# Performance work log

Measured on AMD Instinct MI355X. Metric: run time of the kernel, lower is better.

Reference implementation:

```python
import jax, jax.numpy as jnp
import numpy as np

B_SZ, L_SEQ, D_DATA = 2, 1024, 8
D_CTRL = 256
POLY = 40
N_LAYERS = 2
D_STATE = 16
D_CONV = 4
D_INNER = 1 * D_CTRL          # expand_factor_control = 1
DT_RANK = -(-D_CTRL // 16)    # ceil(d_model/16) = 16
EPS = 1e-5


def setup_inputs() -> dict:
    key = jax.random.key(0)
    ks = jax.random.split(key, 12)
    s = 0.02
    x = jax.random.uniform(ks[0], (B_SZ, L_SEQ, D_DATA), dtype=jnp.float32)
    y = jax.random.uniform(ks[1], (B_SZ, L_SEQ, D_DATA), dtype=jnp.float32)
    return {
        'x': x,
        'y': y,
        # control_proj (note: fed 2*d_data features in structured forward)
        'control_proj_w': jax.random.normal(ks[2], (D_CTRL, 2 * D_DATA)) * s,
        'control_proj_b': jnp.zeros((D_CTRL,), jnp.float32),
        # stacked Mamba layer params (leading dim = n_layers)
        'norm_w': jnp.ones((N_LAYERS, D_CTRL), jnp.float32),
        'in_proj_w': jax.random.normal(ks[3], (N_LAYERS, 2 * D_INNER, D_CTRL)) * s,
        'conv_w': jax.random.normal(ks[4], (N_LAYERS, D_INNER, D_CONV)) * s,
        'conv_b': jnp.zeros((N_LAYERS, D_INNER), jnp.float32),
        'x_proj_w': jax.random.normal(ks[5], (N_LAYERS, DT_RANK + 2 * D_STATE, D_INNER)) * s,
        'dt_proj_w': jax.random.normal(ks[6], (N_LAYERS, D_INNER, DT_RANK)) * s,
        'dt_proj_b': jnp.zeros((N_LAYERS, D_INNER), jnp.float32),
        'A_log': jnp.tile(jnp.log(jnp.arange(1, D_STATE + 1, dtype=jnp.float32))[None, None, :], (N_LAYERS, D_INNER, 1)),
        'D_skip': jnp.ones((N_LAYERS, D_INNER), jnp.float32),
        'out_proj_w': jax.random.normal(ks[7], (N_LAYERS, D_CTRL, D_INNER)) * s,
        # b_net: Linear(d_control, 2*d_data*poly_dim^2)
        'b_net_w': jax.random.normal(ks[8], (2 * D_DATA * POLY * POLY, D_CTRL)) * s,
        'b_net_b': jnp.zeros((2 * D_DATA * POLY * POLY,), jnp.float32),
    }


def _rmsnorm(u, w):
    return u * jax.lax.rsqrt(jnp.mean(u * u, axis=-1, keepdims=True) + EPS) * w


def _causal_conv(u, w, b):
    # u: [B,L,C]; w: [C,K] depthwise causal conv, pad left K-1
    K = w.shape[-1]
    L = u.shape[1]
    up = jnp.pad(u, ((0, 0), (K - 1, 0), (0, 0)))
    acc = jnp.zeros_like(u)
    for k in range(K):  # K=4, fixed small kernel
        acc = acc + up[:, k:k + L, :] * w[:, k]
    return acc + b


def _mamba(u, norm_w, in_proj_w, conv_w, conv_b, x_proj_w, dt_proj_w, dt_proj_b, A_log, D_skip, out_proj_w):
    # mambapy-style stack of residual blocks: u = mixer(rmsnorm(u)) + u
    for i in range(N_LAYERS):
        r = _rmsnorm(u, norm_w[i])
        xz = jnp.einsum('bld,ed->ble', r, in_proj_w[i])          # [B,L,2*di]
        xc, zg = jnp.split(xz, 2, axis=-1)
        xc = jax.nn.silu(_causal_conv(xc, conv_w[i], conv_b[i]))  # [B,L,di]
        dbc = jnp.einsum('bld,ed->ble', xc, x_proj_w[i])          # [B,L,dt_rank+2*ds]
        delta = jax.nn.softplus(jnp.einsum('blr,dr->bld', dbc[..., :DT_RANK], dt_proj_w[i]) + dt_proj_b[i])
        Bm = dbc[..., DT_RANK:DT_RANK + D_STATE]
        Cm = dbc[..., DT_RANK + D_STATE:]
        A = -jnp.exp(A_log[i])                                    # [di,ds]
        dA = jnp.exp(delta[..., None] * A)                        # [B,L,di,ds]
        dBx = delta[..., None] * Bm[:, :, None, :] * xc[..., None]

        def step(h, inp):
            dA_t, dBx_t = inp
            h = dA_t * h + dBx_t
            return h, h

        h0 = jnp.zeros((u.shape[0], D_INNER, D_STATE), u.dtype)
        _, hs = jax.lax.scan(step, h0, (dA.transpose(1, 0, 2, 3), dBx.transpose(1, 0, 2, 3)))
        yv = jnp.einsum('lbds,lbs->bld', hs, Cm.transpose(1, 0, 2)) + D_skip[i] * xc
        yv = yv * jax.nn.silu(zg)
        u = jnp.einsum('bld,ed->ble', yv, out_proj_w[i]) + u
    return u


def _power_mat(z):
    # z ** arange(POLY), built with cumprod (grad-safe at exponent 0)
    ones = jnp.ones(z.shape + (1,), z.dtype)
    reps = jnp.broadcast_to(z[..., None], z.shape + (POLY - 1,))
    return jnp.cumprod(jnp.concatenate([ones, reps], axis=-1), axis=-1)  # [B,L,2d,P]


def reference(x, y, control_proj_w, control_proj_b, norm_w, in_proj_w, conv_w, conv_b,
              x_proj_w, dt_proj_w, dt_proj_b, A_log, D_skip, out_proj_w, b_net_w, b_net_b):
    B, L, d = x.shape
    xdot = y - x
    z = jnp.concatenate([x, xdot], axis=-1)                       # [B,L,2d]
    pm = _power_mat(z)                                            # [B,L,2d,P]
    ctrl_in = jnp.flip(jnp.concatenate([xdot, y], axis=-1), axis=1)
    ctrl_in = ctrl_in @ control_proj_w.T + control_proj_b
    sp = _mamba(ctrl_in, norm_w, in_proj_w, conv_w, conv_b, x_proj_w,
                dt_proj_w, dt_proj_b, A_log, D_skip, out_proj_w)
    state_pred = jnp.flip(sp, axis=1)                             # [B,L,d_ctrl]
    bmat = (state_pred @ b_net_w.T + b_net_b).reshape(B, L, 2 * d, POLY, POLY)
    pow1 = jnp.einsum('bldkj,bldk->bldj', bmat, pm)
    zdot = jnp.einsum('bldj,bldj->bld', pow1, jnp.flip(pm, axis=2))
    return zdot[:, 1:, :], state_pred
```

## Files before the change

### kernel.cpp

```cpp
#include <hip/hip_runtime.h>
#include <hip/hip_bf16.h>

#define B_SZ   2
#define LSEQ   1024
#define DD     8
#define DCTRL  256
#define POLY   40
#define NL     2
#define DSTATE 16
#define DCONV  4
#define DINNER 256
#define DTRANK 16
#define NBL    (B_SZ*LSEQ)
#define NROWS  (2*DD*POLY*POLY)
#define NSLOT  25
#define NCH    32
#define LCH    32
#define LDP    40

typedef __attribute__((ext_vector_type(8))) short bf16x8;
typedef __attribute__((ext_vector_type(8))) unsigned short us8;
typedef __attribute__((ext_vector_type(4))) unsigned short us4;
typedef __attribute__((ext_vector_type(4))) float f32x4;

__device__ __forceinline__ float sigmoidf_(float x){ return 1.f/(1.f+__expf(-x)); }
__device__ __forceinline__ float softplusf_(float x){ return fmaxf(x,0.f) + log1pf(__expf(-fabsf(x))); }
__device__ __forceinline__ unsigned short f2bf(float f){
  unsigned int u = __float_as_uint(f);
  unsigned int r = (u + 0x7fffu + ((u>>16)&1u)) >> 16;
  return (unsigned short)r;
}

__global__ void k_f2bf(const float* __restrict__ in, unsigned short* __restrict__ out, int n8){
  int i = blockIdx.x*blockDim.x + threadIdx.x;
  if (i>=n8) return;
  const float4* p = (const float4*)(in + (size_t)i*8);
  float4 a = p[0], b = p[1];
  us8 r;
  r[0]=f2bf(a.x); r[1]=f2bf(a.y); r[2]=f2bf(a.z); r[3]=f2bf(a.w);
  r[4]=f2bf(b.x); r[5]=f2bf(b.y); r[6]=f2bf(b.z); r[7]=f2bf(b.w);
  *(us8*)(out + (size_t)i*8) = r;
}

#define IPW_N8 (NL*512*256/8)
#define OPW_N8 (NL*256*256/8)
#define PRE_B0 ((IPW_N8+OPW_N8)/256)
#define PRE_B1 (NL*288*256/256)
#define PRE_B2 (16*NBL/256)
#define PRE_B3 (NBL*256/256)
#define PRE_B4 (NROWS*256/8/256)
__global__ void k_prologue(const float* __restrict__ ipw, const float* __restrict__ opw,
                           const float* __restrict__ dtw, const float* __restrict__ xpw,
                           const float* __restrict__ x,   const float* __restrict__ y,
                           const float* __restrict__ cpw, const float* __restrict__ cpb,
                           const float* __restrict__ bnw,
                           unsigned short* __restrict__ ipwb,
                           unsigned short* __restrict__ wcomb,
                           float* __restrict__ pmt, float* __restrict__ u,
                           unsigned short* __restrict__ Wb){
  int bx = blockIdx.x; int tid = threadIdx.x;
  if (bx < PRE_B0){
    int i = bx*256 + tid;
    const float* src = (i < IPW_N8) ? (ipw + (size_t)i*8) : (opw + (size_t)(i-IPW_N8)*8);
    const float4* p = (const float4*)src;
    float4 a = p[0], b = p[1];
    us8 r;
    r[0]=f2bf(a.x); r[1]=f2bf(a.y); r[2]=f2bf(a.z); r[3]=f2bf(a.w);
    r[4]=f2bf(b.x); r[5]=f2bf(b.y); r[6]=f2bf(b.z); r[7]=f2bf(b.w);
    *(us8*)(ipwb + (size_t)i*8) = r;
  } else if (bx < PRE_B0+PRE_B1){
    int idx = (bx-PRE_B0)*256 + tid;
    int e = idx & 255; int row = (idx>>8) % 288; int l = idx / (288*256);
    float v;
    if (row < 256){
      float s=0.f;
      #pragma unroll
      for (int r=0;r<16;++r) s += dtw[((size_t)l*256+row)*16+r] * xpw[((size_t)l*48+r)*256+e];
      v = s;
    } else {
      v = xpw[((size_t)l*48 + (row-240))*256 + e];
    }
    wcomb[idx] = f2bf(v);
  } else if (bx < PRE_B0+PRE_B1+PRE_B2){
    int idx = (bx-PRE_B0-PRE_B1)*256 + tid;
    int m = idx & (NBL-1); int c = idx >> 11;
    float z;
    if (c < 8) z = x[(size_t)m*8 + c];
    else       z = y[(size_t)m*8 + (c-8)] - x[(size_t)m*8 + (c-8)];
    float p = 1.f;
    #pragma unroll
    for (int j=0;j<POLY;++j){ pmt[((size_t)c*POLY+j)*NBL + m] = p; p*=z; }
  } else if (bx < PRE_B0+PRE_B1+PRE_B2+PRE_B3){
    int idx = (bx-PRE_B0-PRE_B1-PRE_B2)*256 + tid;
    int e = idx & 255; int m = idx >> 8;
    int bb = m >> 10; int lm = m & 1023; int lo = 1023 - lm;
    const float* xp = x + ((size_t)bb*1024+lo)*8;
    const float* yp = y + ((size_t)bb*1024+lo)*8;
    const float* wr = cpw + (size_t)e*16;
    float acc = cpb[e];
    #pragma unroll
    for (int d=0; d<8; ++d) acc += (yp[d]-xp[d])*wr[d];
    #pragma unroll
    for (int d=0; d<8; ++d) acc += yp[d]*wr[8+d];
    u[idx] = acc;
  } else {
    int i = (bx-PRE_B0-PRE_B1-PRE_B2-PRE_B3)*256 + tid;
    const float4* p = (const float4*)(bnw + (size_t)i*8);
    float4 a = p[0], b = p[1];
    us8 r;
    r[0]=f2bf(a.x); r[1]=f2bf(a.y); r[2]=f2bf(a.z); r[3]=f2bf(a.w);
    r[4]=f2bf(b.x); r[5]=f2bf(b.y); r[6]=f2bf(b.z); r[7]=f2bf(b.w);
    *(us8*)(Wb + (size_t)i*8) = r;
  }
}

__global__ void k_rms(const float* __restrict__ u, const float* __restrict__ nw,
                      unsigned short* __restrict__ rb){
  int m = blockIdx.x; int e = threadIdx.x;
  float v = u[(size_t)m*256 + e];
  float ss = v*v;
  #pragma unroll
  for (int off=32; off>0; off>>=1) ss += __shfl_down(ss, off);
  __shared__ float sred[4];
  __shared__ float srstd;
  int wid = e>>6; int lane = e&63;
  if (lane==0) sred[wid]=ss;
  __syncthreads();
  if (e==0){ float t = sred[0]+sred[1]+sred[2]+sred[3]; srstd = rsqrtf(t*(1.f/256.f) + 1e-5f); }
  __syncthreads();
  rb[(size_t)m*256+e] = f2bf(v * srstd * nw[e]);
}

__global__ void __launch_bounds__(256)
gemm_bf(const unsigned short* __restrict__ A, const unsigned short* __restrict__ B,
        int N, int K, const float* __restrict__ bias,
        float* __restrict__ C0, float* __restrict__ C1, int ldc, int mode,
        float* __restrict__ outsp, unsigned short* __restrict__ spb){
  __shared__ __align__(16) unsigned short Asm[64*LDP];
  __shared__ __align__(16) unsigned short Bsm[64*LDP];
  int tid = threadIdx.x;
  int lane = tid & 63;
  int w = tid >> 6; int wr = w >> 1, wc = w & 1;
  int l15 = lane & 15, l4 = lane >> 4;
  int m0 = blockIdx.y*64, n0 = blockIdx.x*64;

  f32x4 acc[2][2];
  #pragma unroll
  for (int i=0;i<2;++i)
    #pragma unroll
    for (int j=0;j<2;++j){ acc[i][j][0]=0.f; acc[i][j][1]=0.f; acc[i][j][2]=0.f; acc[i][j][3]=0.f; }

  int row = tid>>2, c8 = tid&3;
  int nks = K >> 5;
  for (int ks=0; ks<nks; ++ks){
    int k0 = ks*32;
    *(us8*)&Asm[row*LDP + c8*8] = *(const us8*)(A + (size_t)(m0+row)*K + k0 + c8*8);
    {
      int bn = n0+row;
      us8 v;
      if (bn < N){
        v = *(const us8*)(B + (size_t)bn*K + k0 + c8*8);
      } else {
        for (int z=0;z<8;++z) v[z]=0;
      }
      *(us8*)&Bsm[row*LDP + c8*8] = v;
    }
    __syncthreads();
    bf16x8 av[2], bv[2];
    #pragma unroll
    for (int i=0;i<2;++i) av[i] = *(bf16x8*)&Asm[(wr*32+i*16+l15)*LDP + l4*8];
    #pragma unroll
    for (int j=0;j<2;++j) bv[j] = *(bf16x8*)&Bsm[(wc*32+j*16+l15)*LDP + l4*8];
    #pragma unroll
    for (int i=0;i<2;++i)
      #pragma unroll
      for (int j=0;j<2;++j)
        acc[i][j] = __builtin_amdgcn_mfma_f32_16x16x32_bf16(av[i], bv[j], acc[i][j], 0,0,0);
    __syncthreads();
  }

  #pragma unroll
  for (int i=0;i<2;++i){
    #pragma unroll
    for (int j=0;j<2;++j){
      int n = n0 + wc*32 + j*16 + l15;
      #pragma unroll
      for (int q=0;q<4;++q){
        int m = m0 + wr*32 + i*16 + l4*4 + q;
        float v = acc[i][j][q];
        if (mode==0){
          C0[(size_t)m*ldc + n] = v;
        } else if (mode==1){
          C0[(size_t)m*ldc + n] += v;
        } else if (mode==2){
          if (n < 256) C0[(size_t)m*256 + n] = softplusf_(v + bias[n]);
          else if (n < N) C1[(size_t)m*32 + (n-256)] = v;
        } else {
          float t = C0[(size_t)m*ldc + n] + v;
          int bb = m >> 10; int lq = m & 1023;
          size_t mf = (size_t)bb*1024 + (1023-lq);
          outsp[mf*256 + n] = t;
          spb[mf*256 + n] = f2bf(t);
        }
      }
    }
  }
}

__global__ void k_convsilu(const float* __restrict__ xz, const float* __restrict__ cw,
                           const float* __restrict__ cb, float* __restrict__ xc,
                           unsigned short* __restrict__ xcb){
  int idx = blockIdx.x*blockDim.x + threadIdx.x;
  if (idx >= NBL*64) return;
  int d4 = (idx & 63) << 2; int m = idx >> 6;
  int bb = m>>10, l = m&1023;
  float4 w0 = *(const float4*)&cw[(d4+0)*4];
  float4 w1 = *(const float4*)&cw[(d4+1)*4];
  float4 w2 = *(const float4*)&cw[(d4+2)*4];
  float4 w3 = *(const float4*)&cw[(d4+3)*4];
  float4 cbv = *(const float4*)&cb[d4];
  float a0=cbv.x, a1=cbv.y, a2=cbv.z, a3=cbv.w;
  #pragma unroll
  for (int k=0;k<4;++k){
    int ls = l - 3 + k;
    if (ls >= 0){
      float4 v = *(const float4*)&xz[((size_t)(bb*1024+ls))*512 + d4];
      a0 += v.x * ((const float*)&w0)[k];
      a1 += v.y * ((const float*)&w1)[k];
      a2 += v.z * ((const float*)&w2)[k];
      a3 += v.w * ((const float*)&w3)[k];
    }
  }
  a0 = a0*sigmoidf_(a0); a1 = a1*sigmoidf_(a1);
  a2 = a2*sigmoidf_(a2); a3 = a3*sigmoidf_(a3);
  float4 o; o.x=a0; o.y=a1; o.z=a2; o.w=a3;
  *(float4*)&xc[(size_t)m*256 + d4] = o;
  us4 ob; ob[0]=f2bf(a0); ob[1]=f2bf(a1); ob[2]=f2bf(a2); ob[3]=f2bf(a3);
  *(us4*)&xcb[(size_t)m*256 + d4] = ob;
}

__global__ void k_scan1(const float* __restrict__ delta, const float* __restrict__ bc,
                        const float* __restrict__ xc, const float* __restrict__ alog,
                        float* __restrict__ hend, float* __restrict__ Pc){
  int blk = blockIdx.x;
  int dg = blk & 15; int ch = (blk>>4) & (NCH-1); int bb = blk >> 9;
  int tid = threadIdx.x; int dl = tid>>4; int s = tid&15; int d = dg*16+dl;
  float A = -__expf(alog[(size_t)d*16+s]);
  float h = 0.f, p = 1.f;
  size_t base = (size_t)bb*1024 + ch*LCH;
  #pragma unroll 4
  for (int t=0;t<LCH;++t){
    size_t mb = base + t;
    float de  = delta[mb*256+d];
    float Bv  = bc[mb*32+s];
    float xcv = xc[mb*256+d];
    float a = __expf(de*A);
    h = a*h + de*Bv*xcv;
    p *= a;
  }
  size_t o = (((size_t)bb*NCH+ch)*256+d)*16+s;
  hend[o]=h; Pc[o]=p;
}

__global__ void k_scan2(const float* __restrict__ hend, const float* __restrict__ Pc,
                        float* __restrict__ Hinit){
  int idx = blockIdx.x*blockDim.x + threadIdx.x;
  if (idx >= B_SZ*256*16) return;
  int bb = idx >> 12; int ds = idx & 4095;
  float H = 0.f;
  #pragma unroll
  for (int ch=0; ch<NCH; ++ch){
    size_t o = ((size_t)bb*NCH+ch)*4096 + ds;
    Hinit[o] = H;
    H = Pc[o]*H + hend[o];
  }
}

__global__ void k_scan3(const float* __restrict__ delta, const float* __restrict__ bc,
                        const float* __restrict__ xc, const float* __restrict__ xz,
                        const float* __restrict__ alog, const float* __restrict__ dskip,
                        const float* __restrict__ Hinit, unsigned short* __restrict__ yvb){
  int blk = blockIdx.x;
  int dg = blk & 15; int ch = (blk>>4) & (NCH-1); int bb = blk >> 9;
  int tid = threadIdx.x; int dl = tid>>4; int s = tid&15; int d = dg*16+dl;
  float A = -__expf(alog[(size_t)d*16+s]);
  float dsk = dskip[d];
  float h = Hinit[(((size_t)bb*NCH+ch)*256+d)*16+s];
  size_t base = (size_t)bb*1024 + ch*LCH;
  #pragma unroll 2
  for (int t=0;t<LCH;++t){
    size_t mb = base + t;
    float de  = delta[mb*256+d];
    float Bv  = bc[mb*32+s];
    float Cv  = bc[mb*32+16+s];
    float xcv = xc[mb*256+d];
    float a = __expf(de*A);
    h = a*h + de*Bv*xcv;
    float yval = h*Cv;
    yval += __shfl_xor(yval,1);
    yval += __shfl_xor(yval,2);
    yval += __shfl_xor(yval,4);
    yval += __shfl_xor(yval,8);
    if (s==0){
      float zg = xz[mb*512+256+d];
      yvb[mb*256+d] = f2bf((yval + dsk*xcv) * zg * sigmoidf_(zg));
    }
  }
}

__global__ void __launch_bounds__(256)
k_bnet_mfma(const unsigned short* __restrict__ spb, const unsigned short* __restrict__ Wb,
            const float* __restrict__ bnb, const float* __restrict__ pmt,
            float* __restrict__ part){
  __shared__ __align__(16) unsigned short Asm[2][128*LDP];
  __shared__ __align__(16) unsigned short Bsm[2][64*LDP];
  __shared__ float red[2][128];

  int tid = threadIdx.x;
  int lane = tid & 63;
  int w = tid >> 6;
  int wr = w >> 1, wc = w & 1;
  int l15 = lane & 15, l4 = lane >> 4;
  int bx = blockIdx.x;
  int m0 = blockIdx.y*128;
  int n0 = bx*64;

  int aRow0 = (tid)>>2,        aC0 = (tid)&3;
  int aRow1 = (tid+256)>>2,    aC1 = (tid+256)&3;
  int bRow  = tid>>2,          bC  = tid&3;
  const unsigned short* aSrc0 = spb + ((size_t)(m0+aRow0))*256 + aC0*8;
  const unsigned short* aSrc1 = spb + ((size_t)(m0+aRow1))*256 + aC1*8;
  const unsigned short* bSrc  = Wb  + ((size_t)(n0+bRow ))*256 + bC*8;

  f32x4 acc[4][2];
  #pragma unroll
  for (int i=0;i<4;++i)
    #pragma unroll
    for (int j=0;j<2;++j){ acc[i][j][0]=0.f; acc[i][j][1]=0.f; acc[i][j][2]=0.f; acc[i][j][3]=0.f; }

  {
    us8 t0 = *(const us8*)(aSrc0);
    us8 t1 = *(const us8*)(aSrc1);
    us8 t2 = *(const us8*)(bSrc);
    *(us8*)&Asm[0][aRow0*LDP + aC0*8] = t0;
    *(us8*)&Asm[0][aRow1*LDP + aC1*8] = t1;
    *(us8*)&Bsm[0][bRow*LDP + bC*8]   = t2;
  }
  us8 pA0 = *(const us8*)(aSrc0 + 32);
  us8 pA1 = *(const us8*)(aSrc1 + 32);
  us8 pB  = *(const us8*)(bSrc  + 32);
  __syncthreads();

  int cur = 0;
  for (int ks=0; ks<8; ++ks){
    us8 qA0, qA1, qB;
    if (ks < 6){
      int k0nn = (ks+2)*32;
      qA0 = *(const us8*)(aSrc0 + k0nn);
      qA1 = *(const us8*)(aSrc1 + k0nn);
      qB  = *(const us8*)(bSrc  + k0nn);
    }
    bf16x8 av[4], bv[2];
    #pragma unroll
    for (int i=0;i<4;++i) av[i] = *(bf16x8*)&Asm[cur][(wr*64+i*16+l15)*LDP + l4*8];
    #pragma unroll
    for (int j=0;j<2;++j) bv[j] = *(bf16x8*)&Bsm[cur][(wc*32+j*16+l15)*LDP + l4*8];
    __builtin_amdgcn_s_setprio(1);
    #pragma unroll
    for (int i=0;i<4;++i)
      #pragma unroll
      for (int j=0;j<2;++j)
        acc[i][j] = __builtin_amdgcn_mfma_f32_16x16x32_bf16(av[i], bv[j], acc[i][j], 0,0,0);
    __builtin_amdgcn_s_setprio(0);
    if (ks < 7){
      *(us8*)&Asm[cur^1][aRow0*LDP + aC0*8] = pA0;
      *(us8*)&Asm[cur^1][aRow1*LDP + aC1*8] = pA1;
      *(us8*)&Bsm[cur^1][bRow*LDP + bC*8]   = pB;
    }
    __syncthreads();
    cur ^= 1;
    if (ks < 6){ pA0 = qA0; pA1 = qA1; pB = qB; }
  }

  int c = bx/25, slot = bx%25;
  int rem0 = slot*64;
  float bnbv[2]; int kkv[2], jjv[2];
  #pragma unroll
  for (int j=0;j<2;++j){
    int nl = wc*32 + j*16 + l15;
    int rem = rem0 + nl;
    bnbv[j] = bnb[n0 + nl];
    kkv[j] = rem/40; jjv[j] = rem%40;
  }
  const float* pc  = pmt + (size_t)c*POLY*NBL;
  const float* pcf = pmt + (size_t)(15-c)*POLY*NBL;
  #pragma unroll
  for (int i=0;i<4;++i){
    int mb = m0 + wr*64 + i*16 + l4*4;
    f32x4 s; s[0]=0.f; s[1]=0.f; s[2]=0.f; s[3]=0.f;
    #pragma unroll
    for (int j=0;j<2;++j){
      f32x4 pk = *(const f32x4*)&pc [(size_t)kkv[j]*NBL + mb];
      f32x4 pj = *(const f32x4*)&pcf[(size_t)jjv[j]*NBL + mb];
      #pragma unroll
      for (int q=0;q<4;++q) s[q] += (acc[i][j][q] + bnbv[j]) * pk[q] * pj[q];
    }
    #pragma unroll
    for (int q=0;q<4;++q){
      float t = s[q];
      t += __shfl_xor(t,1); t += __shfl_xor(t,2);
      t += __shfl_xor(t,4); t += __shfl_xor(t,8);
      if (l15==0) red[wc][wr*64 + i*16 + l4*4 + q] = t;
    }
  }
  __syncthreads();
  if (tid < 128){
    float v = red[0][tid] + red[1][tid];
    part[((size_t)(c*NSLOT + slot))*NBL + m0 + tid] = v;
  }
}

__global__ void k_final(const float* __restrict__ part, float* __restrict__ out){
  int j = blockIdx.x*blockDim.x+threadIdx.x;
  if (j >= 16*2046) return;
  int c = j / 2046; int r = j % 2046;
  int bb = r / 1023; int l = r % 1023 + 1;
  size_t m = (size_t)bb*1024 + l;
  float s = 0.f;
  #pragma unroll
  for (int q=0;q<NSLOT;++q) s += part[((size_t)(c*NSLOT + q))*NBL + m];
  out[((size_t)(bb*1023 + (l-1)))*16 + c] = s;
}

extern "C" void kernel_launch(void* const* d_in, const int* in_sizes, int n_in,
                              void* d_out, int out_size, void* d_ws, size_t ws_size,
                              hipStream_t stream) {
  const float* x    = (const float*)d_in[0];
  const float* y    = (const float*)d_in[1];
  const float* cpw  = (const float*)d_in[2];
  const float* cpb  = (const float*)d_in[3];
  const float* nw   = (const float*)d_in[4];
  const float* ipw  = (const float*)d_in[5];
  const float* cvw  = (const float*)d_in[6];
  const float* cvb  = (const float*)d_in[7];
  const float* xpw  = (const float*)d_in[8];
  const float* dtw  = (const float*)d_in[9];
  const float* dtb  = (const float*)d_in[10];
  const float* alog = (const float*)d_in[11];
  const float* dsk  = (const float*)d_in[12];
  const float* opw  = (const float*)d_in[13];
  const float* bnw  = (const float*)d_in[14];
  const float* bnb  = (const float*)d_in[15];

  float* out      = (float*)d_out;
  float* out_zdot = out;
  float* out_sp   = out + 32736;

  float* ws = (float*)d_ws;
  size_t off = 0;
  float* u     = ws + off; off += (size_t)NBL*256;
  unsigned short* rb = (unsigned short*)(ws + off); off += (size_t)NBL*256/2;
  float* xz    = ws + off; off += (size_t)NBL*512;
  float* xc    = ws + off; off += (size_t)NBL*256;
  unsigned short* xcb = (unsigned short*)(ws + off); off += (size_t)NBL*256/2;
  float* delta = ws + off; off += (size_t)NBL*256;
  float* bcm   = ws + off; off += (size_t)NBL*32;
  unsigned short* yvb = (unsigned short*)(ws + off); off += (size_t)NBL*256/2;
  float* pmt   = ws + off; off += (size_t)NBL*16*POLY;
  float* part  = ws + off; off += (size_t)NSLOT*NBL*16;
  float* hend  = ws + off; off += (size_t)B_SZ*NCH*256*16;
  float* Pc    = ws + off; off += (size_t)B_SZ*NCH*256*16;
  float* Hinit = ws + off; off += (size_t)B_SZ*NCH*256*16;
  unsigned short* spb  = (unsigned short*)(ws + off); off += (size_t)NBL*256/2;
  unsigned short* ipwb = (unsigned short*)(ws + off); off += (size_t)(IPW_N8+OPW_N8)*4;
  unsigned short* wcomb= (unsigned short*)(ws + off); off += (size_t)NL*288*256/2;

  int wbEarly = ((off + (size_t)NROWS*256/2)*sizeof(float) <= ws_size) ? 1 : 0;
  unsigned short* Wb = wbEarly ? (unsigned short*)(ws + off) : (unsigned short*)ws;

  unsigned short* opwb = ipwb + (size_t)IPW_N8*8;

  int preBlocks = PRE_B0+PRE_B1+PRE_B2+PRE_B3 + (wbEarly ? PRE_B4 : 0);
  k_prologue<<<preBlocks, 256, 0, stream>>>(ipw, opw, dtw, xpw, x, y, cpw, cpb, bnw,
                                            ipwb, wcomb, pmt, u, Wb);

  for (int i=0;i<NL;++i){
    k_rms<<<NBL, 256, 0, stream>>>(u, nw + i*256, rb);
    gemm_bf<<<dim3(8,32), 256, 0, stream>>>(rb, ipwb + (size_t)i*512*256, 512, 256,
                                            nullptr, xz, nullptr, 512, 0, nullptr, nullptr);
    k_convsilu<<<(NBL*64+255)/256, 256, 0, stream>>>(xz, cvw + i*256*4, cvb + i*256, xc, xcb);
    gemm_bf<<<dim3(5,32), 256, 0, stream>>>(xcb, wcomb + (size_t)i*288*256, 288, 256,
                                            dtb + i*256, delta, bcm, 256, 2, nullptr, nullptr);
    k_scan1<<<B_SZ*NCH*16, 256, 0, stream>>>(delta, bcm, xc, alog + (size_t)i*256*16, hend, Pc);
    k_scan2<<<(B_SZ*256*16+255)/256, 256, 0, stream>>>(hend, Pc, Hinit);
    k_scan3<<<B_SZ*NCH*16, 256, 0, stream>>>(delta, bcm, xc, xz, alog + (size_t)i*256*16,
                                             dsk + i*256, Hinit, yvb);
    if (i < NL-1){
      gemm_bf<<<dim3(4,32), 256, 0, stream>>>(yvb, opwb + (size_t)i*256*256, 256, 256,
                                              nullptr, u, nullptr, 256, 1, nullptr, nullptr);
    } else {
      gemm_bf<<<dim3(4,32), 256, 0, stream>>>(yvb, opwb + (size_t)i*256*256, 256, 256,
                                              nullptr, u, nullptr, 256, 3, out_sp, spb);
    }
  }

  if (!wbEarly){
    k_f2bf<<<(NROWS*256/8 + 255)/256, 256, 0, stream>>>(bnw, Wb, NROWS*256/8);
  }
  k_bnet_mfma<<<dim3(NROWS/64, NBL/128), 256, 0, stream>>>(spb, Wb, bnb, pmt, part);
  k_final<<<(16*2046+255)/256, 256, 0, stream>>>(part, out_zdot);
}
```

Measured before the change: 222.2 us.

## Double-buffer LDS tiles with register prefetch in bf16 GEMM main loop

Restructures the bf16 MFMA GEMM k-loop to use two LDS buffers per operand and to prefetch global tiles two k-steps ahead into registers. The next tile is written into the alternate buffer after the MFMAs, so each step needs one barrier instead of two. Raised wave priority around the MFMA block is meant to favour matrix issue. The loop now assumes K is 256 (8 steps), which drops generality, and the extra LDS and registers may reduce occupancy.

```diff
diff --git a/kernel.cpp b/kernel.cpp
--- a/kernel.cpp
+++ b/kernel.cpp
@@ -136,8 +136,8 @@
         int N, int K, const float* __restrict__ bias,
         float* __restrict__ C0, float* __restrict__ C1, int ldc, int mode,
         float* __restrict__ outsp, unsigned short* __restrict__ spb){
-  __shared__ __align__(16) unsigned short Asm[64*LDP];
-  __shared__ __align__(16) unsigned short Bsm[64*LDP];
+  __shared__ __align__(16) unsigned short Asm[2][64*LDP];
+  __shared__ __align__(16) unsigned short Bsm[2][64*LDP];
   int tid = threadIdx.x;
   int lane = tid & 63;
   int w = tid >> 6; int wr = w >> 1, wc = w & 1;
@@ -151,32 +151,52 @@
     for (int j=0;j<2;++j){ acc[i][j][0]=0.f; acc[i][j][1]=0.f; acc[i][j][2]=0.f; acc[i][j][3]=0.f; }
 
   int row = tid>>2, c8 = tid&3;
-  int nks = K >> 5;
-  for (int ks=0; ks<nks; ++ks){
-    int k0 = ks*32;
-    *(us8*)&Asm[row*LDP + c8*8] = *(const us8*)(A + (size_t)(m0+row)*K + k0 + c8*8);
-    {
-      int bn = n0+row;
-      us8 v;
-      if (bn < N){
-        v = *(const us8*)(B + (size_t)bn*K + k0 + c8*8);
-      } else {
-        for (int z=0;z<8;++z) v[z]=0;
-      }
-      *(us8*)&Bsm[row*LDP + c8*8] = v;
-    }
-    __syncthreads();
+  int bn = n0+row; int bValid = (bn < N);
+  const unsigned short* aSrc = A + (size_t)(m0+row)*K + c8*8;
+  const unsigned short* bSrc = B + (size_t)(bValid ? bn : 0)*K + c8*8;
+
+  {
+    us8 t0 = *(const us8*)(aSrc);
+    us8 t1;
+    if (bValid) t1 = *(const us8*)(bSrc);
+    else        for (int z=0;z<8;++z) t1[z]=0;
+    *(us8*)&Asm[0][row*LDP + c8*8] = t0;
+    *(us8*)&Bsm[0][row*LDP + c8*8] = t1;
+  }
+  us8 pA = *(const us8*)(aSrc + 32);
+  us8 pB;
+  if (bValid) pB = *(const us8*)(bSrc + 32);
+  else        for (int z=0;z<8;++z) pB[z]=0;
+  __syncthreads();
+
+  int cur = 0;
+  for (int ks=0; ks<8; ++ks){
+    us8 qA, qB;
+    if (ks < 6){
+      int k0nn = (ks+2)*32;
+      qA = *(const us8*)(aSrc + k0nn);
+      if (bValid) qB = *(const us8*)(bSrc + k0nn);
+      else        for (int z=0;z<8;++z) qB[z]=0;
+    }
     bf16x8 av[2], bv[2];
     #pragma unroll
-    for (int i=0;i<2;++i) av[i] = *(bf16x8*)&Asm[(wr*32+i*16+l15)*LDP + l4*8];
-    #pragma unroll
-    for (int j=0;j<2;++j) bv[j] = *(bf16x8*)&Bsm[(wc*32+j*16+l15)*LDP + l4*8];
+    for (int i=0;i<2;++i) av[i] = *(bf16x8*)&Asm[cur][(wr*32+i*16+l15)*LDP + l4*8];
+    #pragma unroll
+    for (int j=0;j<2;++j) bv[j] = *(bf16x8*)&Bsm[cur][(wc*32+j*16+l15)*LDP + l4*8];
+    __builtin_amdgcn_s_setprio(1);
     #pragma unroll
     for (int i=0;i<2;++i)
       #pragma unroll
       for (int j=0;j<2;++j)
         acc[i][j] = __builtin_amdgcn_mfma_f32_16x16x32_bf16(av[i], bv[j], acc[i][j], 0,0,0);
+    __builtin_amdgcn_s_setprio(0);
+    if (ks < 7){
+      *(us8*)&Asm[cur^1][row*LDP + c8*8] = pA;
+      *(us8*)&Bsm[cur^1][row*LDP + c8*8] = pB;
+    }
     __syncthreads();
+    cur ^= 1;
+    if (ks < 6){ pA = qA; pB = qB; }
   }
 
   #pragma unroll
```

New measurement: 212.1 us (median of 2 runs). -4.5%, faster.
